# Kernel optimization log

Measured on AMD Instinct MI355X. Metric: run time of the kernel, lower is better.

The kernel has to match this reference:

```python
import jax, jax.numpy as jnp
import numpy as np

B, L, D = 1, 4096, 1024
H, DH = 16, 64
BASE = 10000.0


def _rope_tables(L, dh, dtype=jnp.float32):
    inv_freq = 1.0 / (BASE ** (jnp.arange(0, dh, 2, dtype=jnp.float32) / dh))
    freqs = jnp.outer(jnp.arange(L, dtype=jnp.float32), inv_freq)  # [L, dh/2]
    return jnp.cos(freqs).astype(dtype), jnp.sin(freqs).astype(dtype)


def _apply_rope(x, cos, sin):
    # x: [B,H,L,dh]; cos/sin: [L,dh/2]
    x1, x2 = x[..., ::2], x[..., 1::2]
    c = cos[None, None]
    s = sin[None, None]
    return jnp.concatenate([x1 * c - x2 * s, x1 * s + x2 * c], axis=-1)


def setup_inputs() -> dict:
    key = jax.random.key(0)
    ks = jax.random.split(key, 5)
    x = jax.random.normal(ks[0], (B, L, D), dtype=jnp.float32)
    mask = jnp.tril(jnp.ones((L, L), dtype=jnp.int32))  # causal 0/1 mask
    sd = 1.0 / np.sqrt(D)
    Wq = jax.random.normal(ks[1], (D, D), dtype=jnp.float32) * sd
    Wk = jax.random.normal(ks[2], (D, D), dtype=jnp.float32) * sd
    Wv = jax.random.normal(ks[3], (D, D), dtype=jnp.float32) * sd
    Wo = jax.random.normal(ks[4], (D, D), dtype=jnp.float32) * sd
    return {"x": x, "mask": mask, "Wq": Wq, "Wk": Wk, "Wv": Wv, "Wo": Wo}


def reference(x, mask, Wq, Wk, Wv, Wo):
    b, l, d = x.shape
    scale = DH ** -0.5
    cos, sin = _rope_tables(l, DH, x.dtype)

    def heads(w):
        return (x @ w.T).reshape(b, l, H, DH).transpose(0, 2, 1, 3)  # [B,H,L,dh]

    q = _apply_rope(heads(Wq), cos, sin)
    k = _apply_rope(heads(Wk), cos, sin)
    v = heads(Wv)

    attn = jnp.einsum('bhqd,bhkd->bhqk', q, k) * scale
    attn = jnp.where(mask[:l, :l] == 0, -jnp.inf, attn)
    attn = jax.nn.softmax(attn, axis=-1)
    out = jnp.einsum('bhqk,bhkd->bhqd', attn, v)
    out = out.transpose(0, 2, 1, 3).reshape(b, l, d)
    return out @ Wo.T
```

## Files before the change

kernel.cpp:

```cpp
#include <hip/hip_runtime.h>
#include <math.h>

#define LSEQ   4096
#define DMODEL 1024
#define NH     16
#define DHEAD  64
#define PSTRIDE 40
#define MASKV  -30000.0f
#define C2SCALE 0.18033688f

typedef __attribute__((ext_vector_type(8))) short  bf16x8;
typedef __attribute__((ext_vector_type(4))) float  floatx4;
typedef unsigned short ushort_t;

#if __has_builtin(__builtin_amdgcn_exp2f)
#define EXP2F __builtin_amdgcn_exp2f
#else
#define EXP2F exp2f
#endif

__device__ __forceinline__ ushort_t f2bf(float x) {
  unsigned u = __builtin_bit_cast(unsigned, x);
  return (ushort_t)((u + 0x7fff + ((u >> 16) & 1)) >> 16);
}
__device__ __forceinline__ unsigned bf16pair(float a, float b) {
  return (unsigned)f2bf(a) | ((unsigned)f2bf(b) << 16);
}
__device__ __forceinline__ unsigned bfpack_trunc(float a, float b) {
  return __builtin_amdgcn_perm(__builtin_bit_cast(unsigned, b),
                               __builtin_bit_cast(unsigned, a), 0x07060302u);
}
__device__ __forceinline__ void gl_lds16(const ushort_t* g, ushort_t* l) {
  __builtin_amdgcn_global_load_lds(
      (const __attribute__((address_space(1))) void*)g,
      (__attribute__((address_space(3))) void*)l, 16, 0, 0);
}

__global__ void rope_table(float2* __restrict__ rope) {
  const int idx = blockIdx.x * 256 + threadIdx.x;
  const int s = idx >> 5, t = idx & 31;
  const double invf = exp((double)t * -0.28782313662425572);
  const double ang = (double)s * invf;
  rope[idx] = make_float2((float)cos(ang), (float)sin(ang));
}

__global__ void cvt_bf16(const float* __restrict__ x,  const float* __restrict__ wq,
                         const float* __restrict__ wk, const float* __restrict__ wv,
                         const float* __restrict__ wo, ushort_t* __restrict__ dst) {
  const size_t e = ((size_t)blockIdx.x * 256 + threadIdx.x) * 4;
  const float* src; size_t off;
  if      (e < (size_t)(4u << 20)) { src = x;  off = e; }
  else if (e < (size_t)(5u << 20)) { src = wq; off = e - (size_t)(4u << 20); }
  else if (e < (size_t)(6u << 20)) { src = wk; off = e - (size_t)(5u << 20); }
  else if (e < (size_t)(7u << 20)) { src = wv; off = e - (size_t)(6u << 20); }
  else                             { src = wo; off = e - (size_t)(7u << 20); }
  const float4 v = *(const float4*)(src + off);
  uint2 p; p.x = bf16pair(v.x, v.y); p.y = bf16pair(v.z, v.w);
  *(uint2*)(dst + e) = p;
}

__global__ __launch_bounds__(512, 2)
void gemm256_qkv(const ushort_t* __restrict__ A, const ushort_t* __restrict__ B,
                 const float2* __restrict__ rope,
                 ushort_t* __restrict__ Qo, ushort_t* __restrict__ Ko,
                 ushort_t* __restrict__ Vo) {
  __shared__ __align__(16) ushort_t smem[65536];
  const int tid  = threadIdx.x;
  const int w    = tid >> 6, lane = tid & 63;
  const int wr   = w >> 2,   wc   = w & 3;
  const int quad = lane >> 4, col = lane & 15;
  const int csw  = col & 7;
  const int i0 = blockIdx.x * 256;
  const int j0 = blockIdx.y * 256;

  const ushort_t* Ab = A + (size_t)i0 * DMODEL;
  const ushort_t* Bb = B + (size_t)j0 * DMODEL;

  const int sr8 = lane >> 3;
  const int sc  = ((lane & 7) ^ sr8) * 8;

  floatx4 acc[8][4];
#pragma unroll
  for (int m = 0; m < 8; ++m)
#pragma unroll
    for (int n = 0; n < 4; ++n) acc[m][n] = (floatx4){0.f, 0.f, 0.f, 0.f};

  auto stageA = [&](int kt, int h) {
    ushort_t* dst = smem + (kt & 1) * 16384 + (h * 128 + w * 8) * 64;
    const ushort_t* src = Ab + (size_t)(h * 128 + w * 8 + sr8) * DMODEL + kt * 64 + sc;
    gl_lds16(src, dst);
    gl_lds16(src + (size_t)64 * DMODEL, dst + 4096);
  };
  auto stageB = [&](int kt, int h) {
    ushort_t* dst = smem + 32768 + (kt & 1) * 16384 + (h * 128 + w * 8) * 64;
    const ushort_t* src = Bb + (size_t)(h * 128 + w * 8 + sr8) * DMODEL + kt * 64 + sc;
    gl_lds16(src, dst);
    gl_lds16(src + (size_t)64 * DMODEL, dst + 4096);
  };

  stageA(0, 0); stageB(0, 0); stageA(0, 1); stageB(0, 1);
  asm volatile("s_waitcnt vmcnt(0)" ::: "memory");
  __builtin_amdgcn_s_barrier();

#pragma unroll 2
  for (int t = 0; t < 16; ++t) {
    const ushort_t* As_ = smem + (t & 1) * 16384;
    const ushort_t* Bs_ = smem + 32768 + (t & 1) * 16384;
    const bool pre = (t + 1 < 16);

    bf16x8 af[4], bfr[4];
#pragma unroll
    for (int n = 0; n < 4; ++n)
      bfr[n] = *(const bf16x8*)(Bs_ + (wc * 64 + n * 16 + col) * 64 + ((quad ^ csw) * 8));
#pragma unroll
    for (int m = 0; m < 4; ++m)
      af[m] = *(const bf16x8*)(As_ + (wr * 128 + m * 16 + col) * 64 + ((quad ^ csw) * 8));
    if (pre) { stageA(t + 1, 0); stageB(t + 1, 0); }
    __builtin_amdgcn_s_setprio(1);
#pragma unroll
    for (int m = 0; m < 4; ++m)
#pragma unroll
      for (int n = 0; n < 4; ++n)
        acc[m][n] = __builtin_amdgcn_mfma_f32_16x16x32_bf16(af[m], bfr[n], acc[m][n], 0, 0, 0);
    __builtin_amdgcn_s_setprio(0);
    __builtin_amdgcn_s_barrier();

#pragma unroll
    for (int m = 0; m < 4; ++m)
      af[m] = *(const bf16x8*)(As_ + (wr * 128 + (m + 4) * 16 + col) * 64 + ((quad ^ csw) * 8));
    if (pre) { stageA(t + 1, 1); stageB(t + 1, 1); }
    __builtin_amdgcn_s_setprio(1);
#pragma unroll
    for (int m = 0; m < 4; ++m)
#pragma unroll
      for (int n = 0; n < 4; ++n)
        acc[m + 4][n] = __builtin_amdgcn_mfma_f32_16x16x32_bf16(af[m], bfr[n], acc[m + 4][n], 0, 0, 0);
    __builtin_amdgcn_s_setprio(0);
    __builtin_amdgcn_s_barrier();

#pragma unroll
    for (int n = 0; n < 4; ++n)
      bfr[n] = *(const bf16x8*)(Bs_ + (wc * 64 + n * 16 + col) * 64 + (((4 + quad) ^ csw) * 8));
#pragma unroll
    for (int m = 0; m < 4; ++m)
      af[m] = *(const bf16x8*)(As_ + (wr * 128 + m * 16 + col) * 64 + (((4 + quad) ^ csw) * 8));
    __builtin_amdgcn_s_setprio(1);
#pragma unroll
    for (int m = 0; m < 4; ++m)
#pragma unroll
      for (int n = 0; n < 4; ++n)
        acc[m][n] = __builtin_amdgcn_mfma_f32_16x16x32_bf16(af[m], bfr[n], acc[m][n], 0, 0, 0);
    __builtin_amdgcn_s_setprio(0);
    __builtin_amdgcn_s_barrier();

#pragma unroll
    for (int m = 0; m < 4; ++m)
      af[m] = *(const bf16x8*)(As_ + (wr * 128 + (m + 4) * 16 + col) * 64 + (((4 + quad) ^ csw) * 8));
    __builtin_amdgcn_s_setprio(1);
#pragma unroll
    for (int m = 0; m < 4; ++m)
#pragma unroll
      for (int n = 0; n < 4; ++n)
        acc[m + 4][n] = __builtin_amdgcn_mfma_f32_16x16x32_bf16(af[m], bfr[n], acc[m + 4][n], 0, 0, 0);
    __builtin_amdgcn_s_setprio(0);
    asm volatile("s_waitcnt vmcnt(0)" ::: "memory");
    __builtin_amdgcn_s_barrier();
  }

  const int which = i0 >> 10;
#pragma unroll
  for (int m = 0; m < 8; ++m) {
    const int f0 = i0 + wr * 128 + m * 16 + quad * 4;
    const int h  = (f0 >> 6) & 15;
    const int d  = f0 & 63;
    if (which == 2) {
#pragma unroll
      for (int n = 0; n < 4; ++n) {
        const int s = j0 + wc * 64 + n * 16 + col;
#pragma unroll
        for (int r = 0; r < 4; ++r)
          Vo[(size_t)(h * DHEAD + d + r) * LSEQ + s] = f2bf(acc[m][n][r]);
      }
    } else {
      ushort_t* dst = which ? Ko : Qo;
      const float qs = which ? 1.0f : C2SCALE;
      const int t0 = d >> 1;
#pragma unroll
      for (int n = 0; n < 4; ++n) {
        const int s = j0 + wc * 64 + n * 16 + col;
        const float4 cst = *(const float4*)((const float*)rope + ((size_t)s << 6) + t0 * 2);
        ushort_t* ob = dst + ((size_t)h * LSEQ + s) * DHEAD;
        const float x1 = acc[m][n][0], x2 = acc[m][n][1];
        const float y1 = acc[m][n][2], y2 = acc[m][n][3];
        *(unsigned*)(ob + t0)      = bf16pair((x1 * cst.x - x2 * cst.y) * qs,
                                              (y1 * cst.z - y2 * cst.w) * qs);
        *(unsigned*)(ob + t0 + 32) = bf16pair((x1 * cst.y + x2 * cst.x) * qs,
                                              (y1 * cst.w + y2 * cst.z) * qs);
      }
    }
  }
}

template<int MODE>
__global__ __launch_bounds__(256)
void mfma_gemm(const ushort_t* __restrict__ A, const ushort_t* __restrict__ B,
               float* __restrict__ C, const float2* __restrict__ rope,
               ushort_t* __restrict__ Qo, ushort_t* __restrict__ Ko,
               ushort_t* __restrict__ Vo) {
  __shared__ ushort_t As[128 * 64];
  __shared__ ushort_t Bs[128 * 64];
  const int tid  = threadIdx.x;
  const int w    = tid >> 6, lane = tid & 63;
  const int wm   = w >> 1,   wn   = w & 1;
  const int quad = lane >> 4, col = lane & 15;
  const int csw  = col & 7;
  const int i0 = blockIdx.x * 128;
  const int j0 = blockIdx.y * 128;

  const ushort_t* Ab = A + (size_t)i0 * DMODEL;
  const ushort_t* Bb = B + (size_t)j0 * DMODEL;

  floatx4 acc[4][4];
#pragma unroll
  for (int mt = 0; mt < 4; ++mt)
#pragma unroll
    for (int nt = 0; nt < 4; ++nt) acc[mt][nt] = (floatx4){0.f, 0.f, 0.f, 0.f};

  const int lrow = lane >> 3;
  const int lcol = ((lane & 7) ^ lrow) * 8;

  for (int k0 = 0; k0 < DMODEL; k0 += 64) {
    __syncthreads();
#pragma unroll
    for (int it = 0; it < 4; ++it) {
      const int rb = (it * 4 + w) * 8;
      gl_lds16(Ab + (size_t)(rb + lrow) * DMODEL + k0 + lcol, As + rb * 64);
      gl_lds16(Bb + (size_t)(rb + lrow) * DMODEL + k0 + lcol, Bs + rb * 64);
    }
    __syncthreads();

#pragma unroll
    for (int kk = 0; kk < 64; kk += 32) {
      const int cblk = (kk >> 3) + quad;
      bf16x8 af[4], bfr[4];
#pragma unroll
      for (int mt = 0; mt < 4; ++mt)
        af[mt] = *(const bf16x8*)(As + (wm * 64 + mt * 16 + col) * 64 +
                                  ((cblk ^ csw) * 8));
#pragma unroll
      for (int nt = 0; nt < 4; ++nt)
        bfr[nt] = *(const bf16x8*)(Bs + (wn * 64 + nt * 16 + col) * 64 +
                                   ((cblk ^ csw) * 8));
#pragma unroll
      for (int mt = 0; mt < 4; ++mt)
#pragma unroll
        for (int nt = 0; nt < 4; ++nt)
          acc[mt][nt] = __builtin_amdgcn_mfma_f32_16x16x32_bf16(
              af[mt], bfr[nt], acc[mt][nt], 0, 0, 0);
    }
  }

  if (MODE == 0) {
#pragma unroll
    for (int mt = 0; mt < 4; ++mt) {
      const int i = i0 + wm * 64 + mt * 16 + quad * 4;
#pragma unroll
      for (int nt = 0; nt < 4; ++nt) {
        const int j = j0 + wn * 64 + nt * 16 + col;
#pragma unroll
        for (int r = 0; r < 4; ++r)
          C[(size_t)(i + r) * DMODEL + j] = acc[mt][nt][r];
      }
    }
  } else {
    const int which = i0 >> 10;
#pragma unroll
    for (int mt = 0; mt < 4; ++mt) {
      const int f0 = i0 + wm * 64 + mt * 16 + quad * 4;
      const int h  = (f0 >> 6) & 15;
      const int d  = f0 & 63;
      if (which == 2) {
#pragma unroll
        for (int nt = 0; nt < 4; ++nt) {
          const int s = j0 + wn * 64 + nt * 16 + col;
#pragma unroll
          for (int r = 0; r < 4; ++r)
            Vo[(size_t)(h * DHEAD + d + r) * LSEQ + s] = f2bf(acc[mt][nt][r]);
        }
      } else {
        ushort_t* dst = which ? Ko : Qo;
        const float qs = which ? 1.0f : C2SCALE;
        const int t0 = d >> 1;
#pragma unroll
        for (int nt = 0; nt < 4; ++nt) {
          const int s = j0 + wn * 64 + nt * 16 + col;
          const float4 cst = *(const float4*)((const float*)rope + ((size_t)s << 6) + t0 * 2);
          ushort_t* ob = dst + ((size_t)h * LSEQ + s) * DHEAD;
          const float x1 = acc[mt][nt][0], x2 = acc[mt][nt][1];
          const float y1 = acc[mt][nt][2], y2 = acc[mt][nt][3];
          *(unsigned*)(ob + t0)      = bf16pair((x1 * cst.x - x2 * cst.y) * qs,
                                                (y1 * cst.z - y2 * cst.w) * qs);
          *(unsigned*)(ob + t0 + 32) = bf16pair((x1 * cst.y + x2 * cst.x) * qs,
                                                (y1 * cst.w + y2 * cst.z) * qs);
        }
      }
    }
  }
}

__global__ __launch_bounds__(1024, 4)
void attn_mfma(const ushort_t* __restrict__ Qh, const ushort_t* __restrict__ Kh,
               const ushort_t* __restrict__ Vt, ushort_t* __restrict__ Om) {
  const int h   = blockIdx.x;
  const int g   = blockIdx.y;
  const int tid = threadIdx.x;
  const int w     = tid >> 6;
  const int wl    = w & 3;
  const int half  = (w >> 2) & 1;
  const int ktpar = w >> 3;
  const int wg    = w & 7;
  const int lane = tid & 63;
  const int quad = lane >> 4;
  const int col  = lane & 15;
  const int csw  = col & 7;

  __shared__ __align__(16) char smem[106496];
  ushort_t* Ks   = (ushort_t*)smem;
  ushort_t* Vs   = (ushort_t*)(smem + 32768);
  ushort_t* Ps   = (ushort_t*)(smem + 65536);
  float*    Obuf = (float*)smem;
  __shared__ float lbuf[3][4][2][16];
  ushort_t* psw = Ps + w * (32 * PSTRIDE);

  const int srow = wg * 8 + (lane >> 3);
  const int scol = (((lane & 7) ^ ((lane >> 3) & 7)) * 8);

  for (int pass = 0; pass < 2; ++pass) {
    const int qb      = pass ? (31 - g) : g;
    const int qbase   = qb * 128 + wl * 32;
    const int nkt_max = 2 * qb + 2;
    const int nt2     = nkt_max >> 1;

    bf16x8 qf[2][2];
#pragma unroll
    for (int nq = 0; nq < 2; ++nq)
#pragma unroll
      for (int c = 0; c < 2; ++c)
        qf[nq][c] = *(const bf16x8*)(Qh +
            ((size_t)(h * LSEQ + qbase + nq * 16 + col)) * DHEAD + quad * 8 + c * 32);

    floatx4 ot[4][2];
#pragma unroll
    for (int md = 0; md < 4; ++md)
#pragma unroll
      for (int nq = 0; nq < 2; ++nq) ot[md][nq] = (floatx4){0.f, 0.f, 0.f, 0.f};
    float l_[2] = {0.f, 0.f};

    auto stage = [&](int kt, int b) {
      const int key0 = kt * 64;
      const int boff = (ktpar * 2 + b) * 4096;
      gl_lds16(Kh + ((size_t)(h * LSEQ + key0 + srow)) * DHEAD + scol,
               Ks + boff + wg * 512);
      gl_lds16(Vt + ((size_t)(h * DHEAD + srow)) * LSEQ + key0 + scol,
               Vs + boff + wg * 512);
    };

    stage(ktpar, 0);
    __syncthreads();

    for (int ktt = 0; ktt < nt2; ++ktt) {
      const int kt  = 2 * ktt + ktpar;
      const int buf = ktt & 1;
      if (ktt + 1 < nt2) stage(kt + 2, buf ^ 1);

      const ushort_t* kb = Ks + (ktpar * 2 + buf) * 4096;
      const ushort_t* vb = Vs + (ktpar * 2 + buf) * 4096;

      bf16x8 kf[2][2];
#pragma unroll
      for (int mk = 0; mk < 2; ++mk)
#pragma unroll
        for (int c = 0; c < 2; ++c)
          kf[mk][c] = *(const bf16x8*)(kb + (half * 32 + mk * 16 + col) * 64 +
                                       (((c * 4 + quad) ^ csw) * 8));

      floatx4 st[2][2];
#pragma unroll
      for (int mk = 0; mk < 2; ++mk)
#pragma unroll
        for (int nq = 0; nq < 2; ++nq) st[mk][nq] = (floatx4){0.f, 0.f, 0.f, 0.f};
#pragma unroll
      for (int mk = 0; mk < 2; ++mk)
#pragma unroll
        for (int c = 0; c < 2; ++c)
#pragma unroll
          for (int nq = 0; nq < 2; ++nq)
            st[mk][nq] = __builtin_amdgcn_mfma_f32_16x16x32_bf16(
                kf[mk][c], qf[nq][c], st[mk][nq], 0, 0, 0);

      if (kt >= nkt_max - 2) {
        const int key0 = kt * 64 + half * 32;
#pragma unroll
        for (int mk = 0; mk < 2; ++mk) {
          const int keyb = key0 + mk * 16 + quad * 4;
#pragma unroll
          for (int nq = 0; nq < 2; ++nq) {
            const int q = qbase + nq * 16 + col;
#pragma unroll
            for (int r = 0; r < 4; ++r)
              if (keyb + r > q) st[mk][nq][r] = MASKV;
          }
        }
      }

#pragma unroll
      for (int mk = 0; mk < 2; ++mk)
#pragma unroll
        for (int nq = 0; nq < 2; ++nq) {
#pragma unroll
          for (int r = 0; r < 4; ++r) st[mk][nq][r] = EXP2F(st[mk][nq][r]);
          l_[nq] += (st[mk][nq][0] + st[mk][nq][1]) + (st[mk][nq][2] + st[mk][nq][3]);
        }

#pragma unroll
      for (int mk = 0; mk < 2; ++mk)
#pragma unroll
        for (int nq = 0; nq < 2; ++nq) {
          uint2 pk;
          pk.x = bfpack_trunc(st[mk][nq][0], st[mk][nq][1]);
          pk.y = bfpack_trunc(st[mk][nq][2], st[mk][nq][3]);
          *(uint2*)(psw + (nq * 16 + col) * PSTRIDE + mk * 16 + quad * 4) = pk;
        }
      bf16x8 pf[2];
#pragma unroll
      for (int nq = 0; nq < 2; ++nq)
        pf[nq] = *(const bf16x8*)(psw + (nq * 16 + col) * PSTRIDE + quad * 8);

      bf16x8 vf[4];
#pragma unroll
      for (int md = 0; md < 4; ++md)
        vf[md] = *(const bf16x8*)(vb + (md * 16 + col) * 64 +
                                  (((half * 4 + quad) ^ csw) * 8));
#pragma unroll
      for (int md = 0; md < 4; ++md)
#pragma unroll
        for (int nq = 0; nq < 2; ++nq)
          ot[md][nq] = __builtin_amdgcn_mfma_f32_16x16x32_bf16(
              vf[md], pf[nq], ot[md][nq], 0, 0, 0);

      __syncthreads();
    }

    float lr[2];
#pragma unroll
    for (int nq = 0; nq < 2; ++nq) {
      float ls = l_[nq];
      ls += __shfl_xor(ls, 16);
      ls += __shfl_xor(ls, 32);
      lr[nq] = ls;
    }

    const int di = ((half << 1) | ktpar) - 1;
    if (di >= 0) {
#pragma unroll
      for (int nq = 0; nq < 2; ++nq) {
        if (quad == 0) lbuf[di][wl][nq][col] = lr[nq];
#pragma unroll
        for (int md = 0; md < 4; ++md)
          *(float4*)(Obuf + di * 8704 + ((wl * 2 + nq) * 16 + col) * 68 + md * 16 + quad * 4) =
              (float4){ot[md][nq][0], ot[md][nq][1], ot[md][nq][2], ot[md][nq][3]};
      }
    }
    __syncthreads();

    if (di < 0) {
#pragma unroll
      for (int nq = 0; nq < 2; ++nq) {
        const float inv = 1.0f / (lr[nq] + lbuf[0][wl][nq][col] +
                                  lbuf[1][wl][nq][col] + lbuf[2][wl][nq][col]);
        const int q = qbase + nq * 16 + col;
#pragma unroll
        for (int md = 0; md < 4; ++md) {
          const int ob_off = ((wl * 2 + nq) * 16 + col) * 68 + md * 16 + quad * 4;
          const float4 o0 = *(const float4*)(Obuf + ob_off);
          const float4 o1 = *(const float4*)(Obuf + 8704 + ob_off);
          const float4 o2 = *(const float4*)(Obuf + 17408 + ob_off);
          uint2 pk;
          pk.x = bf16pair((ot[md][nq][0] + o0.x + o1.x + o2.x) * inv,
                          (ot[md][nq][1] + o0.y + o1.y + o2.y) * inv);
          pk.y = bf16pair((ot[md][nq][2] + o0.z + o1.z + o2.z) * inv,
                          (ot[md][nq][3] + o0.w + o1.w + o2.w) * inv);
          *(uint2*)(Om + (size_t)q * DMODEL + h * DHEAD + md * 16 + quad * 4) = pk;
        }
      }
    }
    __syncthreads();
  }
}

extern "C" void kernel_launch(void* const* d_in, const int* in_sizes, int n_in,
                              void* d_out, int out_size, void* d_ws, size_t ws_size,
                              hipStream_t stream) {
  const float* x  = (const float*)d_in[0];
  const float* Wq = (const float*)d_in[2];
  const float* Wk = (const float*)d_in[3];
  const float* Wv = (const float*)d_in[4];
  const float* Wo = (const float*)d_in[5];
  float* out = (float*)d_out;

  const size_t M1 = (size_t)1 << 20;
  ushort_t* xb  = (ushort_t*)d_ws;
  ushort_t* Wb  = xb  + 4 * M1;
  ushort_t* wob = Wb  + 3 * M1;
  ushort_t* Qh  = wob + 1 * M1;
  ushort_t* Kh  = Qh  + 4 * M1;
  ushort_t* Vt  = Kh  + 4 * M1;
  ushort_t* Om  = Vt  + 4 * M1;
  float2*   rope = (float2*)(Om + 4 * M1);

  rope_table<<<512, 256, 0, stream>>>(rope);
  cvt_bf16<<<8192, 256, 0, stream>>>(x, Wq, Wk, Wv, Wo, xb);
  gemm256_qkv<<<dim3(3072 / 256, LSEQ / 256), 512, 0, stream>>>(
      Wb, xb, rope, Qh, Kh, Vt);
  attn_mfma<<<dim3(NH, 16), 1024, 0, stream>>>(Qh, Kh, Vt, Om);
  mfma_gemm<0><<<dim3(LSEQ / 128, DMODEL / 128), 256, 0, stream>>>(
      Om, wob, out, nullptr, nullptr, nullptr, nullptr);
}
```

Before: 239.5 us.

## Load K and V fragments directly from global memory instead of LDS staging

Removes the double-buffered global-to-LDS staging of K and V tiles in the attention kernel. Each wave now reads its K and V MFMA fragments straight from global memory, and the per-iteration block barrier is dropped. The V load is issued before the masking and softmax work to hide its latency. This removes LDS traffic and block-wide synchronization, but every wave now fetches its own K/V data, relying on L1/L2 caching and adding global load latency. LDS is relaid out so P and Obuf no longer overlap, which increases shared memory use.

```diff
diff --git a/kernel.cpp b/kernel.cpp
--- a/kernel.cpp
+++ b/kernel.cpp
@@ -318,22 +318,15 @@
   const int wl    = w & 3;
   const int half  = (w >> 2) & 1;
   const int ktpar = w >> 3;
-  const int wg    = w & 7;
   const int lane = tid & 63;
   const int quad = lane >> 4;
   const int col  = lane & 15;
-  const int csw  = col & 7;
-
-  __shared__ __align__(16) char smem[106496];
-  ushort_t* Ks   = (ushort_t*)smem;
-  ushort_t* Vs   = (ushort_t*)(smem + 32768);
-  ushort_t* Ps   = (ushort_t*)(smem + 65536);
-  float*    Obuf = (float*)smem;
+
+  __shared__ __align__(16) char smem[145408];
+  ushort_t* Ps   = (ushort_t*)smem;
+  float*    Obuf = (float*)(smem + 40960);
   __shared__ float lbuf[3][4][2][16];
   ushort_t* psw = Ps + w * (32 * PSTRIDE);
-
-  const int srow = wg * 8 + (lane >> 3);
-  const int scol = (((lane & 7) ^ ((lane >> 3) & 7)) * 8);
 
   for (int pass = 0; pass < 2; ++pass) {
     const int qb      = pass ? (31 - g) : g;
@@ -356,33 +349,18 @@
       for (int nq = 0; nq < 2; ++nq) ot[md][nq] = (floatx4){0.f, 0.f, 0.f, 0.f};
     float l_[2] = {0.f, 0.f};
 
-    auto stage = [&](int kt, int b) {
-      const int key0 = kt * 64;
-      const int boff = (ktpar * 2 + b) * 4096;
-      gl_lds16(Kh + ((size_t)(h * LSEQ + key0 + srow)) * DHEAD + scol,
-               Ks + boff + wg * 512);
-      gl_lds16(Vt + ((size_t)(h * DHEAD + srow)) * LSEQ + key0 + scol,
-               Vs + boff + wg * 512);
-    };
-
-    stage(ktpar, 0);
-    __syncthreads();
+    const ushort_t* Kp = Kh + ((size_t)(h * LSEQ + ktpar * 64 + half * 32)) * DHEAD;
+    const ushort_t* Vp = Vt + ((size_t)h * DHEAD) * LSEQ + ktpar * 64 + half * 32;
 
     for (int ktt = 0; ktt < nt2; ++ktt) {
-      const int kt  = 2 * ktt + ktpar;
-      const int buf = ktt & 1;
-      if (ktt + 1 < nt2) stage(kt + 2, buf ^ 1);
-
-      const ushort_t* kb = Ks + (ktpar * 2 + buf) * 4096;
-      const ushort_t* vb = Vs + (ktpar * 2 + buf) * 4096;
+      const int kt = 2 * ktt + ktpar;
 
       bf16x8 kf[2][2];
 #pragma unroll
       for (int mk = 0; mk < 2; ++mk)
 #pragma unroll
         for (int c = 0; c < 2; ++c)
-          kf[mk][c] = *(const bf16x8*)(kb + (half * 32 + mk * 16 + col) * 64 +
-                                       (((c * 4 + quad) ^ csw) * 8));
+          kf[mk][c] = *(const bf16x8*)(Kp + (mk * 16 + col) * DHEAD + c * 32 + quad * 8);
 
       floatx4 st[2][2];
 #pragma unroll
@@ -397,6 +375,11 @@
           for (int nq = 0; nq < 2; ++nq)
             st[mk][nq] = __builtin_amdgcn_mfma_f32_16x16x32_bf16(
                 kf[mk][c], qf[nq][c], st[mk][nq], 0, 0, 0);
+
+      bf16x8 vf[4];
+#pragma unroll
+      for (int md = 0; md < 4; ++md)
+        vf[md] = *(const bf16x8*)(Vp + (size_t)(md * 16 + col) * LSEQ + quad * 8);
 
       if (kt >= nkt_max - 2) {
         const int key0 = kt * 64 + half * 32;
@@ -436,11 +419,6 @@
       for (int nq = 0; nq < 2; ++nq)
         pf[nq] = *(const bf16x8*)(psw + (nq * 16 + col) * PSTRIDE + quad * 8);
 
-      bf16x8 vf[4];
-#pragma unroll
-      for (int md = 0; md < 4; ++md)
-        vf[md] = *(const bf16x8*)(vb + (md * 16 + col) * 64 +
-                                  (((half * 4 + quad) ^ csw) * 8));
 #pragma unroll
       for (int md = 0; md < 4; ++md)
 #pragma unroll
@@ -448,7 +426,8 @@
           ot[md][nq] = __builtin_amdgcn_mfma_f32_16x16x32_bf16(
               vf[md], pf[nq], ot[md][nq], 0, 0, 0);
 
-      __syncthreads();
+      Kp += (size_t)128 * DHEAD;
+      Vp += 128;
     }
 
     float lr[2];
```

Result: slower. 311.4 us (+30.0%).
